# Kernel tuning notes

Measured on AMD Instinct MI355X. Metric: run time of the kernel, lower is better.

## Reference

```python
import jax, jax.numpy as jnp
import numpy as np
import math

D_MODEL = 1024
D_STATE = 16
D_CONV = 4
EXPAND = 2
D_INNER = EXPAND * D_MODEL
DT_RANK = math.ceil(D_MODEL / 16)
EPS = 1e-5


def setup_inputs() -> dict:
    key = jax.random.key(0)
    ks = jax.random.split(key, 8)
    B, L = 2, 1024
    s = 0.02
    return {
        "hidden_states": jax.random.normal(ks[0], (B, L, D_MODEL), jnp.float32),
        "norm_weight": jnp.ones((D_MODEL,), jnp.float32),
        "in_proj_w": (jax.random.normal(ks[1], (2 * D_INNER, D_MODEL), jnp.float32) * s),
        "conv_w": (jax.random.normal(ks[2], (D_INNER, D_CONV), jnp.float32) * s),
        "conv_b": jnp.zeros((D_INNER,), jnp.float32),
        "x_proj_w": (jax.random.normal(ks[3], (DT_RANK + 2 * D_STATE, D_INNER), jnp.float32) * s),
        "dt_proj_w": (jax.random.normal(ks[4], (D_INNER, DT_RANK), jnp.float32) * s),
        "dt_proj_b": jax.random.uniform(ks[5], (D_INNER,), jnp.float32, -4.0, -2.0),
        "A_log": jnp.log(jnp.broadcast_to(jnp.arange(1, D_STATE + 1, dtype=jnp.float32), (D_INNER, D_STATE))),
        "D": jnp.ones((D_INNER,), jnp.float32),
        "out_proj_w": (jax.random.normal(ks[6], (D_MODEL, D_INNER), jnp.float32) * s),
    }


def _rmsnorm(x, w):
    # Faithful to source: rms = ||x||_2 / sqrt(d); x / (rms + eps) * w
    norm = jnp.linalg.norm(x, axis=-1, keepdims=True)
    rms = norm * (1.0 / math.sqrt(x.shape[-1]))
    return w * (x / (rms + EPS))


def _mamba(h, in_proj_w, conv_w, conv_b, x_proj_w, dt_proj_w, dt_proj_b, A_log, D, out_proj_w):
    B, L, _ = h.shape
    xz = h @ in_proj_w.T                      # (B,L,2*D_INNER)
    x, z = jnp.split(xz, 2, axis=-1)          # each (B,L,D_INNER)

    # causal depthwise conv1d along L, kernel D_CONV
    xpad = jnp.pad(x, ((0, 0), (D_CONV - 1, 0), (0, 0)))
    xc = conv_b
    for k in range(D_CONV):                   # tiny fixed loop over kernel taps
        xc = xc + xpad[:, k:k + L, :] * conv_w[:, k]
    xc = jax.nn.silu(xc)                      # (B,L,D_INNER)

    x_dbl = xc @ x_proj_w.T                   # (B,L,DT_RANK+2N)
    dt, Bm, Cm = jnp.split(x_dbl, [DT_RANK, DT_RANK + D_STATE], axis=-1)
    dt = jax.nn.softplus(dt @ dt_proj_w.T + dt_proj_b)   # (B,L,D_INNER)

    A = -jnp.exp(A_log)                       # (D_INNER,N)
    deltaA = jnp.exp(dt[..., None] * A)                      # (B,L,D_INNER,N)
    deltaBu = (dt * xc)[..., None] * Bm[:, :, None, :]        # (B,L,D_INNER,N)

    def step(hst, inp):
        dA, dBu, Ct = inp
        hst = dA * hst + dBu                  # (B,D_INNER,N)
        y = jnp.einsum('bdn,bn->bd', hst, Ct)
        return hst, y

    h0 = jnp.zeros((B, D_INNER, D_STATE), xc.dtype)
    _, ys = jax.lax.scan(step, h0, (deltaA.swapaxes(0, 1), deltaBu.swapaxes(0, 1), Cm.swapaxes(0, 1)))
    y = ys.swapaxes(0, 1)                     # (B,L,D_INNER)
    y = y + D * xc
    y = y * jax.nn.silu(z)
    return y @ out_proj_w.T                   # (B,L,D_MODEL)


def reference(hidden_states, norm_weight, in_proj_w, conv_w, conv_b, x_proj_w,
              dt_proj_w, dt_proj_b, A_log, D, out_proj_w):
    residual = hidden_states
    h = _rmsnorm(residual, norm_weight)
    out = _mamba(h, in_proj_w, conv_w, conv_b, x_proj_w, dt_proj_w, dt_proj_b,
                 A_log, D, out_proj_w)
    return out, residual
```

## Files before the change

### kernel.cpp

```cpp
#include <hip/hip_runtime.h>

typedef __bf16 bf16x8 __attribute__((ext_vector_type(8)));
typedef float f32x4 __attribute__((ext_vector_type(4)));

__device__ __forceinline__ float b2f(ushort u) {
    union { unsigned int i; float f; } v;
    v.i = ((unsigned int)u) << 16;
    return v.f;
}
__device__ __forceinline__ ushort f2b(float f) {
    union { float f; unsigned int i; } v;
    v.f = f;
    unsigned int x = v.i;
    unsigned int r = (x + 0x7fffu + ((x >> 16) & 1u)) >> 16;
    return (ushort)r;
}

#define D_MODEL 1024
#define D_INNER 2048
#define D_STATE 16
#define DT_RANK 64
#define NTOK    2048
#define LSEQ    1024
#define NCH     32
#define LC      32
#define KSL     16

__global__ __launch_bounds__(256) void cvt_bf16_kernel(
    const float* __restrict__ src, ushort* __restrict__ dst, int n4)
{
    int i = blockIdx.x * 256 + threadIdx.x;
    if (i >= n4) return;
    float4 v = *(const float4*)(src + i * 4);
    ushort4 o;
    o.x = f2b(v.x); o.y = f2b(v.y); o.z = f2b(v.z); o.w = f2b(v.w);
    *(ushort4*)(dst + i * 4) = o;
}

__global__ __launch_bounds__(256) void rmsnorm_kernel(
    const float* __restrict__ hs, const float* __restrict__ w,
    ushort* __restrict__ hout, float* __restrict__ resid)
{
    int t = blockIdx.x;
    int tid = threadIdx.x;
    float4 r4 = *(const float4*)(hs + (size_t)t * D_MODEL + tid * 4);
    float s = r4.x * r4.x + r4.y * r4.y + r4.z * r4.z + r4.w * r4.w;
    #pragma unroll
    for (int off = 32; off >= 1; off >>= 1) s += __shfl_xor(s, off);
    __shared__ float red[4];
    int lane = tid & 63, wid = tid >> 6;
    if (lane == 0) red[wid] = s;
    __syncthreads();
    float tot = red[0] + red[1] + red[2] + red[3];
    float inv = 1.0f / (sqrtf(tot) * (1.0f / 32.0f) + 1e-5f);
    float4 w4 = *(const float4*)(w + tid * 4);
    ushort4 o;
    o.x = f2b(w4.x * r4.x * inv);
    o.y = f2b(w4.y * r4.y * inv);
    o.z = f2b(w4.z * r4.z * inv);
    o.w = f2b(w4.w * r4.w * inv);
    *(ushort4*)(hout + (size_t)t * D_MODEL + tid * 4) = o;
    *(float4*)(resid + (size_t)t * D_MODEL + tid * 4) = r4;
}

__global__ __launch_bounds__(256) void gemm_bt_kernel(
    const ushort* __restrict__ Ag, const ushort* __restrict__ Wg,
    float* __restrict__ Cf, int M, int N, int K)
{
    __shared__ __align__(16) ushort sA[128 * 40];
    __shared__ __align__(16) ushort sB[128 * 40];
    int tid = threadIdx.x;
    int bm = blockIdx.x, bn = blockIdx.y;
    int wid = tid >> 6, lane = tid & 63;
    int wm = (wid >> 1) * 64, wn = (wid & 1) * 64;
    int l16 = lane & 15, q = lane >> 4;

    f32x4 acc[4][4];
    #pragma unroll
    for (int i = 0; i < 4; i++)
        #pragma unroll
        for (int j = 0; j < 4; j++)
            acc[i][j] = (f32x4){0.f, 0.f, 0.f, 0.f};

    const ushort* Abase = Ag + (size_t)bm * 128 * K;
    const ushort* Wbase = Wg + (size_t)bn * 128 * K;

    int r0 = tid >> 2, c0 = (tid & 3) << 3;
    const ushort* pA0 = Abase + (size_t)r0 * K + c0;
    const ushort* pA1 = Abase + (size_t)(r0 + 64) * K + c0;
    const ushort* pB0 = Wbase + (size_t)r0 * K + c0;
    const ushort* pB1 = Wbase + (size_t)(r0 + 64) * K + c0;

    uint4 pa0 = *(const uint4*)(pA0), pa1 = *(const uint4*)(pA1);
    uint4 pb0 = *(const uint4*)(pB0), pb1 = *(const uint4*)(pB1);

    for (int k0 = 0; k0 < K; k0 += 32) {
        *(uint4*)(sA + r0 * 40 + c0)        = pa0;
        *(uint4*)(sA + (r0 + 64) * 40 + c0) = pa1;
        *(uint4*)(sB + r0 * 40 + c0)        = pb0;
        *(uint4*)(sB + (r0 + 64) * 40 + c0) = pb1;
        __syncthreads();
        if (k0 + 32 < K) {
            pa0 = *(const uint4*)(pA0 + k0 + 32);
            pa1 = *(const uint4*)(pA1 + k0 + 32);
            pb0 = *(const uint4*)(pB0 + k0 + 32);
            pb1 = *(const uint4*)(pB1 + k0 + 32);
        }
        bf16x8 af[4], bfr[4];
        #pragma unroll
        for (int i = 0; i < 4; i++)
            af[i] = *(const bf16x8*)(sA + (wm + i * 16 + l16) * 40 + q * 8);
        #pragma unroll
        for (int j = 0; j < 4; j++)
            bfr[j] = *(const bf16x8*)(sB + (wn + j * 16 + l16) * 40 + q * 8);
        #pragma unroll
        for (int i = 0; i < 4; i++)
            #pragma unroll
            for (int j = 0; j < 4; j++)
                acc[i][j] = __builtin_amdgcn_mfma_f32_16x16x32_bf16(af[i], bfr[j], acc[i][j], 0, 0, 0);
        __syncthreads();
    }

    int row0 = bm * 128 + wm + q * 4;
    int col0 = bn * 128 + wn + l16;
    #pragma unroll
    for (int i = 0; i < 4; i++)
        #pragma unroll
        for (int j = 0; j < 4; j++)
            #pragma unroll
            for (int r = 0; r < 4; r++)
                Cf[(size_t)(row0 + i * 16 + r) * N + col0 + j * 16] = acc[i][j][r];
}

__global__ __launch_bounds__(256) void gemm64_kernel(
    const ushort* __restrict__ Ag, const ushort* __restrict__ Wg,
    float* __restrict__ Cf, int M, int N, int K)
{
    __shared__ __align__(16) ushort sA[64 * 72];
    __shared__ __align__(16) ushort sB[64 * 72];
    int tid = threadIdx.x;
    int bm = blockIdx.x, bn = blockIdx.y;
    int wid = tid >> 6, lane = tid & 63;
    int wm = wid * 16;
    int l16 = lane & 15, q = lane >> 4;

    f32x4 acc[4];
    #pragma unroll
    for (int j = 0; j < 4; j++) acc[j] = (f32x4){0.f, 0.f, 0.f, 0.f};

    const ushort* Abase = Ag + (size_t)bm * 64 * K;
    const ushort* Wbase = Wg + (size_t)bn * 64 * K;

    int r0 = tid >> 3, c0 = (tid & 7) << 3;
    const ushort* pA0 = Abase + (size_t)r0 * K + c0;
    const ushort* pA1 = Abase + (size_t)(r0 + 32) * K + c0;
    const ushort* pB0 = Wbase + (size_t)r0 * K + c0;
    const ushort* pB1 = Wbase + (size_t)(r0 + 32) * K + c0;

    uint4 pa0 = *(const uint4*)(pA0), pa1 = *(const uint4*)(pA1);
    uint4 pb0 = *(const uint4*)(pB0), pb1 = *(const uint4*)(pB1);

    for (int k0 = 0; k0 < K; k0 += 64) {
        *(uint4*)(sA + r0 * 72 + c0)        = pa0;
        *(uint4*)(sA + (r0 + 32) * 72 + c0) = pa1;
        *(uint4*)(sB + r0 * 72 + c0)        = pb0;
        *(uint4*)(sB + (r0 + 32) * 72 + c0) = pb1;
        __syncthreads();
        if (k0 + 64 < K) {
            pa0 = *(const uint4*)(pA0 + k0 + 64);
            pa1 = *(const uint4*)(pA1 + k0 + 64);
            pb0 = *(const uint4*)(pB0 + k0 + 64);
            pb1 = *(const uint4*)(pB1 + k0 + 64);
        }
        #pragma unroll
        for (int ks = 0; ks < 2; ks++) {
            bf16x8 af = *(const bf16x8*)(sA + (wm + l16) * 72 + ks * 32 + q * 8);
            bf16x8 bfr[4];
            #pragma unroll
            for (int j = 0; j < 4; j++)
                bfr[j] = *(const bf16x8*)(sB + (j * 16 + l16) * 72 + ks * 32 + q * 8);
            #pragma unroll
            for (int j = 0; j < 4; j++)
                acc[j] = __builtin_amdgcn_mfma_f32_16x16x32_bf16(af, bfr[j], acc[j], 0, 0, 0);
        }
        __syncthreads();
    }

    int row0 = bm * 64 + wm + q * 4;
    int col0 = bn * 64 + l16;
    #pragma unroll
    for (int j = 0; j < 4; j++)
        #pragma unroll
        for (int r = 0; r < 4; r++)
            Cf[(size_t)(row0 + r) * N + col0 + j * 16] = acc[j][r];
}

__global__ __launch_bounds__(256) void conv_silu_kernel(
    const float* __restrict__ xz, const float* __restrict__ cw,
    const float* __restrict__ cb, float* __restrict__ xc, ushort* __restrict__ xcb)
{
    int idx = blockIdx.x * 256 + threadIdx.x;
    int d = idx & (D_INNER - 1);
    int t = idx >> 11;
    int l = t & (LSEQ - 1), b = t >> 10;
    float4 w4 = *(const float4*)(cw + d * 4);
    float acc = cb[d];
    float wk[4] = {w4.x, w4.y, w4.z, w4.w};
    #pragma unroll
    for (int k = 0; k < 4; k++) {
        int ll = l - 3 + k;
        float xv = (ll >= 0) ? xz[(((size_t)(b * LSEQ + ll)) << 12) + d] : 0.f;
        acc += xv * wk[k];
    }
    float sg = acc / (1.f + __expf(-acc));
    xc[idx] = sg;
    xcb[idx] = f2b(sg);
}

__global__ __launch_bounds__(256) void xproj_partial_kernel(
    const ushort* __restrict__ xcb, const ushort* __restrict__ wq,
    float* __restrict__ partials)
{
    __shared__ __align__(16) ushort sA[128 * 32];
    __shared__ __align__(16) ushort sB[96 * 32];
    int tid = threadIdx.x;
    int bm = blockIdx.x, sl = blockIdx.y;
    int wid = tid >> 6, lane = tid & 63;
    int wm = wid * 32;
    int l16 = lane & 15, q = lane >> 4;

    f32x4 acc[2][6];
    #pragma unroll
    for (int i = 0; i < 2; i++)
        #pragma unroll
        for (int j = 0; j < 6; j++)
            acc[i][j] = (f32x4){0.f, 0.f, 0.f, 0.f};

    const ushort* Abase = xcb + (size_t)bm * 128 * D_INNER;
    int kbase = sl * (D_INNER / KSL);

    for (int kk = 0; kk < D_INNER / KSL; kk += 32) {
        int k0 = kbase + kk;
        __syncthreads();
        #pragma unroll
        for (int i = tid; i < 512; i += 256) {
            int r = i >> 2, c = (i & 3) << 3;
            *(uint4*)(sA + i * 8) = *(const uint4*)(Abase + (size_t)r * D_INNER + k0 + c);
        }
        for (int i = tid; i < 384; i += 256) {
            int r = i >> 2, c = (i & 3) << 3;
            *(uint4*)(sB + i * 8) = *(const uint4*)(wq + (size_t)r * D_INNER + k0 + c);
        }
        __syncthreads();
        bf16x8 af[2], bfr[6];
        #pragma unroll
        for (int i = 0; i < 2; i++)
            af[i] = *(const bf16x8*)(sA + (wm + i * 16 + l16) * 32 + q * 8);
        #pragma unroll
        for (int j = 0; j < 6; j++)
            bfr[j] = *(const bf16x8*)(sB + (j * 16 + l16) * 32 + q * 8);
        #pragma unroll
        for (int i = 0; i < 2; i++)
            #pragma unroll
            for (int j = 0; j < 6; j++)
                acc[i][j] = __builtin_amdgcn_mfma_f32_16x16x32_bf16(af[i], bfr[j], acc[i][j], 0, 0, 0);
    }

    float* out = partials + (size_t)sl * NTOK * 96;
    int row0 = bm * 128 + wm + q * 4;
    #pragma unroll
    for (int i = 0; i < 2; i++)
        #pragma unroll
        for (int j = 0; j < 6; j++)
            #pragma unroll
            for (int r = 0; r < 4; r++)
                out[(size_t)(row0 + i * 16 + r) * 96 + j * 16 + l16] = acc[i][j][r];
}

__global__ __launch_bounds__(256) void xproj_reduce_kernel(
    const float* __restrict__ partials, float* __restrict__ xdbl,
    ushort* __restrict__ xdbl64)
{
    int idx = blockIdx.x * 256 + threadIdx.x;
    float s = 0.f;
    #pragma unroll
    for (int sl = 0; sl < KSL; sl++)
        s += partials[(size_t)sl * NTOK * 96 + idx];
    xdbl[idx] = s;
    int col = idx % 96;
    if (col < DT_RANK)
        xdbl64[(size_t)(idx / 96) * DT_RANK + col] = f2b(s);
}

__global__ __launch_bounds__(256) void dt_gemm_kernel(
    const ushort* __restrict__ xd64, const ushort* __restrict__ dtwq,
    const float* __restrict__ dtb, ushort* __restrict__ dtout)
{
    __shared__ __align__(16) ushort sA[64 * 72];
    __shared__ __align__(16) ushort sB[64 * 72];
    int tid = threadIdx.x;
    int bm = blockIdx.x, bn = blockIdx.y;
    int wid = tid >> 6, lane = tid & 63;
    int wm = wid * 16;
    int l16 = lane & 15, q = lane >> 4;

    const ushort* Abase = xd64 + (size_t)bm * 64 * DT_RANK;
    const ushort* Bbase = dtwq + (size_t)bn * 64 * DT_RANK;
    #pragma unroll
    for (int i = tid; i < 512; i += 256) {
        int r = i >> 3, c = (i & 7) << 3;
        *(uint4*)(sA + r * 72 + c) = *(const uint4*)(Abase + (size_t)r * DT_RANK + c);
        *(uint4*)(sB + r * 72 + c) = *(const uint4*)(Bbase + (size_t)r * DT_RANK + c);
    }
    __syncthreads();

    f32x4 acc[4];
    #pragma unroll
    for (int j = 0; j < 4; j++) acc[j] = (f32x4){0.f, 0.f, 0.f, 0.f};

    #pragma unroll
    for (int ks = 0; ks < 2; ks++) {
        bf16x8 af = *(const bf16x8*)(sA + (wm + l16) * 72 + ks * 32 + q * 8);
        bf16x8 bfr[4];
        #pragma unroll
        for (int j = 0; j < 4; j++)
            bfr[j] = *(const bf16x8*)(sB + (j * 16 + l16) * 72 + ks * 32 + q * 8);
        #pragma unroll
        for (int j = 0; j < 4; j++)
            acc[j] = __builtin_amdgcn_mfma_f32_16x16x32_bf16(af, bfr[j], acc[j], 0, 0, 0);
    }

    __syncthreads();
    #pragma unroll
    for (int j = 0; j < 4; j++) {
        float bias = dtb[bn * 64 + j * 16 + l16];
        #pragma unroll
        for (int r = 0; r < 4; r++) {
            float s = acc[j][r] + bias;
            float sp = (s > 20.f) ? s : log1pf(__expf(s));
            sA[(wm + q * 4 + r) * 72 + j * 16 + l16] = f2b(sp);
        }
    }
    __syncthreads();
    int row0 = bm * 64, col0 = bn * 64;
    #pragma unroll
    for (int rep = 0; rep < 2; rep++) {
        int off = rep * 2048 + tid * 8;
        int row = off >> 6, col = off & 63;
        *(uint4*)(dtout + (size_t)(row0 + row) * D_INNER + col0 + col) =
            *(const uint4*)(sA + row * 72 + col);
    }
}

__global__ __launch_bounds__(256) void scan_partA_kernel(
    const ushort* __restrict__ dt, const float* __restrict__ xc,
    const float* __restrict__ xdbl, const float* __restrict__ Alog,
    float2* __restrict__ ch1, float2* __restrict__ ch2)
{
    __shared__ float sBC[LC][32];
    int bid = blockIdx.x;
    int g = bid & 7;
    int c = (bid >> 3) & (NCH - 1);
    int b = bid >> 8;
    int tid = threadIdx.x;
    int lane = tid & 63, wid = tid >> 6;
    int d = g * 256 + wid * 64 + lane;
    int l0 = c * LC;

    {
        int r = tid >> 3, c4 = (tid & 7) * 4;
        *(float4*)&sBC[r][c4] =
            *(const float4*)(xdbl + ((size_t)(b * LSEQ + l0 + r)) * 96 + 64 + c4);
    }
    float A[16];
    #pragma unroll
    for (int k = 0; k < 4; k++)
        *(float4*)&A[k * 4] = *(const float4*)(Alog + d * D_STATE + k * 4);
    #pragma unroll
    for (int n = 0; n < 16; n++) A[n] = -__expf(A[n]);
    __syncthreads();

    const ushort* dtp = dt + ((size_t)(b * LSEQ + l0)) * D_INNER + d;
    const float*  xcp = xc + ((size_t)(b * LSEQ + l0)) * D_INNER + d;

    float h[16], ap[16];
    #pragma unroll
    for (int n = 0; n < 16; n++) { h[n] = 0.f; ap[n] = 1.f; }

    for (int l = 0; l < LC; l++) {
        float dtv = b2f(dtp[(size_t)l * D_INNER]);
        float xcv = xcp[(size_t)l * D_INNER];
        float t = dtv * xcv;
        float Bv[16];
        #pragma unroll
        for (int k = 0; k < 4; k++)
            *(float4*)&Bv[k * 4] = *(const float4*)&sBC[l][k * 4];
        #pragma unroll
        for (int n = 0; n < 16; n++) {
            float a = __expf(dtv * A[n]);
            h[n] = h[n] * a + t * Bv[n];
            ap[n] *= a;
        }
    }

    float2* outp = (c < 16 ? ch1 : ch2) +
                   ((size_t)((b * 16 + (c & 15)) * D_INNER + d)) * D_STATE;
    #pragma unroll
    for (int n = 0; n < 16; n += 2) {
        float4 v = {ap[n], h[n], ap[n + 1], h[n + 1]};
        *(float4*)&outp[n] = v;
    }
}

__global__ __launch_bounds__(256) void scan_partB_kernel(
    float2* __restrict__ ch1, float2* __restrict__ ch2)
{
    int kk = blockIdx.x * 256 + threadIdx.x;
    int b = kk >> 15, dn = kk & 32767;
    float run = 0.f;
    #pragma unroll
    for (int c = 0; c < NCH; c++) {
        float2* p = (c < 16 ? ch1 : ch2) +
                    (size_t)(b * 16 + (c & 15)) * 32768 + dn;
        float2 v = *p;
        p->x = run;
        run = v.x * run + v.y;
    }
}

__global__ __launch_bounds__(256) void scan_partC_kernel(
    const ushort* __restrict__ dt, const float* __restrict__ xc,
    const float* __restrict__ xdbl, const float* __restrict__ xz,
    const float* __restrict__ Alog, const float* __restrict__ Dp,
    const float2* __restrict__ ch1, const float2* __restrict__ ch2,
    ushort* __restrict__ yg)
{
    __shared__ float sBC[LC][32];
    int bid = blockIdx.x;
    int g = bid & 7;
    int c = (bid >> 3) & (NCH - 1);
    int b = bid >> 8;
    int tid = threadIdx.x;
    int lane = tid & 63, wid = tid >> 6;
    int d = g * 256 + wid * 64 + lane;
    int l0 = c * LC;

    {
        int r = tid >> 3, c4 = (tid & 7) * 4;
        *(float4*)&sBC[r][c4] =
            *(const float4*)(xdbl + ((size_t)(b * LSEQ + l0 + r)) * 96 + 64 + c4);
    }
    float A[16];
    #pragma unroll
    for (int k = 0; k < 4; k++)
        *(float4*)&A[k * 4] = *(const float4*)(Alog + d * D_STATE + k * 4);
    #pragma unroll
    for (int n = 0; n < 16; n++) A[n] = -__expf(A[n]);
    float Dd = Dp[d];

    const float2* hip_ = (c < 16 ? ch1 : ch2) +
                         ((size_t)((b * 16 + (c & 15)) * D_INNER + d)) * D_STATE;
    float h[16];
    #pragma unroll
    for (int n = 0; n < 16; n += 2) {
        float4 v = *(const float4*)&hip_[n];
        h[n] = v.x; h[n + 1] = v.z;
    }
    __syncthreads();

    const ushort* dtp = dt + ((size_t)(b * LSEQ + l0)) * D_INNER + d;
    const float*  xcp = xc + ((size_t)(b * LSEQ + l0)) * D_INNER + d;
    const float*  zp  = xz + ((size_t)(b * LSEQ + l0)) * (2 * D_INNER) + D_INNER + d;
    ushort* yp = yg + ((size_t)(b * LSEQ + l0)) * D_INNER + d;

    for (int l = 0; l < LC; l++) {
        float dtv = b2f(dtp[(size_t)l * D_INNER]);
        float xcv = xcp[(size_t)l * D_INNER];
        float zv  = zp[(size_t)l * (2 * D_INNER)];
        float t = dtv * xcv;
        float Bv[16], Cv[16];
        #pragma unroll
        for (int k = 0; k < 4; k++) {
            *(float4*)&Bv[k * 4] = *(const float4*)&sBC[l][k * 4];
            *(float4*)&Cv[k * 4] = *(const float4*)&sBC[l][16 + k * 4];
        }
        float p0 = 0.f, p1 = 0.f, p2 = 0.f, p3 = 0.f;
        #pragma unroll
        for (int n = 0; n < 16; n += 4) {
            float a0 = __expf(dtv * A[n]);
            float a1 = __expf(dtv * A[n + 1]);
            float a2 = __expf(dtv * A[n + 2]);
            float a3 = __expf(dtv * A[n + 3]);
            h[n]     = h[n] * a0 + t * Bv[n];
            h[n + 1] = h[n + 1] * a1 + t * Bv[n + 1];
            h[n + 2] = h[n + 2] * a2 + t * Bv[n + 2];
            h[n + 3] = h[n + 3] * a3 + t * Bv[n + 3];
            p0 += h[n] * Cv[n];
            p1 += h[n + 1] * Cv[n + 1];
            p2 += h[n + 2] * Cv[n + 2];
            p3 += h[n + 3] * Cv[n + 3];
        }
        float p = (p0 + p1) + (p2 + p3);
        float y = p + Dd * xcv;
        float sz = zv / (1.f + __expf(-zv));
        yp[(size_t)l * D_INNER] = f2b(y * sz);
    }
}

extern "C" void kernel_launch(void* const* d_in, const int* in_sizes, int n_in,
                              void* d_out, int out_size, void* d_ws, size_t ws_size,
                              hipStream_t stream)
{
    const float* hs      = (const float*)d_in[0];
    const float* norm_w  = (const float*)d_in[1];
    const float* inproj  = (const float*)d_in[2];
    const float* convw   = (const float*)d_in[3];
    const float* convb   = (const float*)d_in[4];
    const float* xprojw  = (const float*)d_in[5];
    const float* dtw     = (const float*)d_in[6];
    const float* dtb     = (const float*)d_in[7];
    const float* alog    = (const float*)d_in[8];
    const float* dvec    = (const float*)d_in[9];
    const float* outproj = (const float*)d_in[10];

    float* out_main  = (float*)d_out;
    float* out_resid = (float*)d_out + (size_t)NTOK * D_MODEL;

    char* ws = (char*)d_ws;
    float*  xz_f32  = (float*)(ws);
    float*  xc_f32  = (float*)(ws + 33554432);
    ushort* dt_bf16 = (ushort*)(ws + 50331648);
    float2* ch1     = (float2*)(ws + 58720256);
    float*  xdbl    = (float*)(ws + 67108864);
    ushort* h_bf16  = (ushort*)(ws + 67895296);
    ushort* yg_bf16 = (ushort*)(ws + 72089600);
    float2* ch2     = (float2*)(ws + 80478208);
    ushort* wIn     = (ushort*)(ws + 80478208);
    ushort* wOut    = (ushort*)(ws + 88866816);
    ushort* xpw_b   = (ushort*)(ws + 67895296);
    ushort* dtw_b   = (ushort*)(ws + 68288512);
    ushort* xd64_b  = (ushort*)(ws + 68550656);
    ushort* xc_bf16 = (ushort*)(ws + 72089600);
    float*  xprojP  = (float*)(ws + 50331648);

    cvt_bf16_kernel<<<(2 * D_INNER * D_MODEL / 4 + 255) / 256, 256, 0, stream>>>(
        inproj, wIn, 2 * D_INNER * D_MODEL / 4);
    cvt_bf16_kernel<<<(D_MODEL * D_INNER / 4 + 255) / 256, 256, 0, stream>>>(
        outproj, wOut, D_MODEL * D_INNER / 4);

    rmsnorm_kernel<<<NTOK, 256, 0, stream>>>(hs, norm_w, h_bf16, out_resid);

    gemm_bt_kernel<<<dim3(NTOK / 128, (2 * D_INNER) / 128), 256, 0, stream>>>(
        h_bf16, wIn, xz_f32, NTOK, 2 * D_INNER, D_MODEL);

    cvt_bf16_kernel<<<(96 * D_INNER / 4 + 255) / 256, 256, 0, stream>>>(
        xprojw, xpw_b, 96 * D_INNER / 4);
    cvt_bf16_kernel<<<(D_INNER * DT_RANK / 4 + 255) / 256, 256, 0, stream>>>(
        dtw, dtw_b, D_INNER * DT_RANK / 4);

    conv_silu_kernel<<<(NTOK * D_INNER) / 256, 256, 0, stream>>>(
        xz_f32, convw, convb, xc_f32, xc_bf16);

    xproj_partial_kernel<<<dim3(NTOK / 128, KSL), 256, 0, stream>>>(
        xc_bf16, xpw_b, xprojP);
    xproj_reduce_kernel<<<NTOK * 96 / 256, 256, 0, stream>>>(xprojP, xdbl, xd64_b);

    dt_gemm_kernel<<<dim3(NTOK / 64, D_INNER / 64), 256, 0, stream>>>(
        xd64_b, dtw_b, dtb, dt_bf16);

    scan_partA_kernel<<<512, 256, 0, stream>>>(dt_bf16, xc_f32, xdbl, alog, ch1, ch2);
    scan_partB_kernel<<<256, 256, 0, stream>>>(ch1, ch2);
    scan_partC_kernel<<<512, 256, 0, stream>>>(dt_bf16, xc_f32, xdbl, xz_f32,
                                               alog, dvec, ch1, ch2, yg_bf16);

    gemm64_kernel<<<dim3(NTOK / 64, D_MODEL / 64), 256, 0, stream>>>(
        yg_bf16, wOut, out_main, NTOK, D_MODEL, D_INNER);
}
```

Baseline: 268.6 us.

## Store xz and conv output in bf16 and merge weight conversion launches

The in-projection GEMM now writes x and z as separate bf16 arrays instead of one fp32 xz buffer. The conv kernel reads bf16 x and emits only the bf16 activation, and both scan kernels read bf16 xc and z. This roughly halves the activation memory traffic between stages and removes the fp32 xc copy. The four weight conversion launches are merged into one kernel. The trade-off is extra rounding error on x, z and xc, and the workspace layout is reorganized.

```diff
diff --git a/kernel.cpp b/kernel.cpp
--- a/kernel.cpp
+++ b/kernel.cpp
@@ -26,15 +26,23 @@
 #define LC      32
 #define KSL     16
 
-__global__ __launch_bounds__(256) void cvt_bf16_kernel(
-    const float* __restrict__ src, ushort* __restrict__ dst, int n4)
+__global__ __launch_bounds__(256) void cvt_all_kernel(
+    const float* __restrict__ inproj, const float* __restrict__ outproj,
+    const float* __restrict__ xprojw, const float* __restrict__ dtw,
+    ushort* __restrict__ wIn, ushort* __restrict__ wOut,
+    ushort* __restrict__ xpw, ushort* __restrict__ dtwb)
 {
     int i = blockIdx.x * 256 + threadIdx.x;
-    if (i >= n4) return;
-    float4 v = *(const float4*)(src + i * 4);
+    const float* src; ushort* dst; int off;
+    if (i < 1048576)      { src = inproj;  dst = wIn;  off = i; }
+    else if (i < 1572864) { src = outproj; dst = wOut; off = i - 1048576; }
+    else if (i < 1622016) { src = xprojw;  dst = xpw;  off = i - 1572864; }
+    else if (i < 1654784) { src = dtw;     dst = dtwb; off = i - 1622016; }
+    else return;
+    float4 v = *(const float4*)(src + (size_t)off * 4);
     ushort4 o;
     o.x = f2b(v.x); o.y = f2b(v.y); o.z = f2b(v.z); o.w = f2b(v.w);
-    *(ushort4*)(dst + i * 4) = o;
+    *(ushort4*)(dst + (size_t)off * 4) = o;
 }
 
 __global__ __launch_bounds__(256) void rmsnorm_kernel(
@@ -63,9 +71,9 @@
     *(float4*)(resid + (size_t)t * D_MODEL + tid * 4) = r4;
 }
 
-__global__ __launch_bounds__(256) void gemm_bt_kernel(
+__global__ __launch_bounds__(256) void gemm_xz_kernel(
     const ushort* __restrict__ Ag, const ushort* __restrict__ Wg,
-    float* __restrict__ Cf, int M, int N, int K)
+    ushort* __restrict__ xq, ushort* __restrict__ zq, int K)
 {
     __shared__ __align__(16) ushort sA[128 * 40];
     __shared__ __align__(16) ushort sB[128 * 40];
@@ -121,15 +129,17 @@
         __syncthreads();
     }
 
+    ushort* dst = (bn < 16) ? xq : zq;
     int row0 = bm * 128 + wm + q * 4;
-    int col0 = bn * 128 + wn + l16;
+    int col0 = (bn & 15) * 128 + wn + l16;
     #pragma unroll
     for (int i = 0; i < 4; i++)
         #pragma unroll
         for (int j = 0; j < 4; j++)
             #pragma unroll
             for (int r = 0; r < 4; r++)
-                Cf[(size_t)(row0 + i * 16 + r) * N + col0 + j * 16] = acc[i][j][r];
+                dst[(size_t)(row0 + i * 16 + r) * D_INNER + col0 + j * 16] =
+                    f2b(acc[i][j][r]);
 }
 
 __global__ __launch_bounds__(256) void gemm64_kernel(
@@ -196,8 +206,8 @@
 }
 
 __global__ __launch_bounds__(256) void conv_silu_kernel(
-    const float* __restrict__ xz, const float* __restrict__ cw,
-    const float* __restrict__ cb, float* __restrict__ xc, ushort* __restrict__ xcb)
+    const ushort* __restrict__ xq, const float* __restrict__ cw,
+    const float* __restrict__ cb, ushort* __restrict__ xcb)
 {
     int idx = blockIdx.x * 256 + threadIdx.x;
     int d = idx & (D_INNER - 1);
@@ -209,11 +219,10 @@
     #pragma unroll
     for (int k = 0; k < 4; k++) {
         int ll = l - 3 + k;
-        float xv = (ll >= 0) ? xz[(((size_t)(b * LSEQ + ll)) << 12) + d] : 0.f;
+        float xv = (ll >= 0) ? b2f(xq[(((size_t)(b * LSEQ + ll)) << 11) + d]) : 0.f;
         acc += xv * wk[k];
     }
     float sg = acc / (1.f + __expf(-acc));
-    xc[idx] = sg;
     xcb[idx] = f2b(sg);
 }
 
@@ -353,7 +362,7 @@
 }
 
 __global__ __launch_bounds__(256) void scan_partA_kernel(
-    const ushort* __restrict__ dt, const float* __restrict__ xc,
+    const ushort* __restrict__ dt, const ushort* __restrict__ xcq,
     const float* __restrict__ xdbl, const float* __restrict__ Alog,
     float2* __restrict__ ch1, float2* __restrict__ ch2)
 {
@@ -380,8 +389,8 @@
     for (int n = 0; n < 16; n++) A[n] = -__expf(A[n]);
     __syncthreads();
 
-    const ushort* dtp = dt + ((size_t)(b * LSEQ + l0)) * D_INNER + d;
-    const float*  xcp = xc + ((size_t)(b * LSEQ + l0)) * D_INNER + d;
+    const ushort* dtp = dt  + ((size_t)(b * LSEQ + l0)) * D_INNER + d;
+    const ushort* xcp = xcq + ((size_t)(b * LSEQ + l0)) * D_INNER + d;
 
     float h[16], ap[16];
     #pragma unroll
@@ -389,7 +398,7 @@
 
     for (int l = 0; l < LC; l++) {
         float dtv = b2f(dtp[(size_t)l * D_INNER]);
-        float xcv = xcp[(size_t)l * D_INNER];
+        float xcv = b2f(xcp[(size_t)l * D_INNER]);
         float t = dtv * xcv;
         float Bv[16];
         #pragma unroll
@@ -429,8 +438,8 @@
 }
 
 __global__ __launch_bounds__(256) void scan_partC_kernel(
-    const ushort* __restrict__ dt, const float* __restrict__ xc,
-    const float* __restrict__ xdbl, const float* __restrict__ xz,
+    const ushort* __restrict__ dt, const ushort* __restrict__ xcq,
+    const float* __restrict__ xdbl, const ushort* __restrict__ zq,
     const float* __restrict__ Alog, const float* __restrict__ Dp,
     const float2* __restrict__ ch1, const float2* __restrict__ ch2,
     ushort* __restrict__ yg)
@@ -468,15 +477,15 @@
     }
     __syncthreads();
 
-    const ushort* dtp = dt + ((size_t)(b * LSEQ + l0)) * D_INNER + d;
-    const float*  xcp = xc + ((size_t)(b * LSEQ + l0)) * D_INNER + d;
-    const float*  zp  = xz + ((size_t)(b * LSEQ + l0)) * (2 * D_INNER) + D_INNER + d;
+    const ushort* dtp = dt  + ((size_t)(b * LSEQ + l0)) * D_INNER + d;
+    const ushort* xcp = xcq + ((size_t)(b * LSEQ + l0)) * D_INNER + d;
+    const ushort* zp  = zq  + ((size_t)(b * LSEQ + l0)) * D_INNER + d;
     ushort* yp = yg + ((size_t)(b * LSEQ + l0)) * D_INNER + d;
 
     for (int l = 0; l < LC; l++) {
         float dtv = b2f(dtp[(size_t)l * D_INNER]);
-        float xcv = xcp[(size_t)l * D_INNER];
-        float zv  = zp[(size_t)l * (2 * D_INNER)];
+        float xcv = b2f(xcp[(size_t)l * D_INNER]);
+        float zv  = b2f(zp[(size_t)l * D_INNER]);
         float t = dtv * xcv;
         float Bv[16], Cv[16];
         #pragma unroll
@@ -527,50 +536,45 @@
     float* out_resid = (float*)d_out + (size_t)NTOK * D_MODEL;
 
     char* ws = (char*)d_ws;
-    float*  xz_f32  = (float*)(ws);
-    float*  xc_f32  = (float*)(ws + 33554432);
-    ushort* dt_bf16 = (ushort*)(ws + 50331648);
-    float2* ch1     = (float2*)(ws + 58720256);
-    float*  xdbl    = (float*)(ws + 67108864);
-    ushort* h_bf16  = (ushort*)(ws + 67895296);
-    ushort* yg_bf16 = (ushort*)(ws + 72089600);
-    float2* ch2     = (float2*)(ws + 80478208);
-    ushort* wIn     = (ushort*)(ws + 80478208);
-    ushort* wOut    = (ushort*)(ws + 88866816);
-    ushort* xpw_b   = (ushort*)(ws + 67895296);
-    ushort* dtw_b   = (ushort*)(ws + 68288512);
-    ushort* xd64_b  = (ushort*)(ws + 68550656);
-    ushort* xc_bf16 = (ushort*)(ws + 72089600);
-    float*  xprojP  = (float*)(ws + 50331648);
-
-    cvt_bf16_kernel<<<(2 * D_INNER * D_MODEL / 4 + 255) / 256, 256, 0, stream>>>(
-        inproj, wIn, 2 * D_INNER * D_MODEL / 4);
-    cvt_bf16_kernel<<<(D_MODEL * D_INNER / 4 + 255) / 256, 256, 0, stream>>>(
-        outproj, wOut, D_MODEL * D_INNER / 4);
+    ushort* xq      = (ushort*)(ws);
+    ushort* zq      = (ushort*)(ws +  9437184);
+    ushort* xcb     = (ushort*)(ws + 18874368);
+    ushort* dtq     = (ushort*)(ws + 28311552);
+    float2* ch1     = (float2*)(ws + 37748736);
+    float2* ch2     = (float2*)(ws + 47185920);
+    float*  xdbl    = (float*) (ws + 56623104);
+    ushort* xd64    = (ushort*)(ws + 57671680);
+    ushort* xpw_b   = (ushort*)(ws + 58195968);
+    ushort* dtw_b   = (ushort*)(ws + 58720256);
+    ushort* wIn     = (ushort*)(ws + 59768832);
+    ushort* wOut    = (ushort*)(ws + 69206016);
+    ushort* h_bf16  = (ushort*)(ws + 74448896);
+    ushort* yg_bf16 = (ushort*)(ws + 18874368);
+    float*  xprojP  = (float*) (ws + 79691776);
+
+    yg_bf16 = (ushort*)(ws + 79691776);
+
+    cvt_all_kernel<<<6464, 256, 0, stream>>>(
+        inproj, outproj, xprojw, dtw, wIn, wOut, xpw_b, dtw_b);
 
     rmsnorm_kernel<<<NTOK, 256, 0, stream>>>(hs, norm_w, h_bf16, out_resid);
 
-    gemm_bt_kernel<<<dim3(NTOK / 128, (2 * D_INNER) / 128), 256, 0, stream>>>(
-        h_bf16, wIn, xz_f32, NTOK, 2 * D_INNER, D_MODEL);
-
-    cvt_bf16_kernel<<<(96 * D_INNER / 4 + 255) / 256, 256, 0, stream>>>(
-        xprojw, xpw_b, 96 * D_INNER / 4);
-    cvt_bf16_kernel<<<(D_INNER * DT_RANK / 4 + 255) / 256, 256, 0, stream>>>(
-        dtw, dtw_b, D_INNER * DT_RANK / 4);
+    gemm_xz_kernel<<<dim3(NTOK / 128, (2 * D_INNER) / 128), 256, 0, stream>>>(
+        h_bf16, wIn, xq, zq, D_MODEL);
 
     conv_silu_kernel<<<(NTOK * D_INNER) / 256, 256, 0, stream>>>(
-        xz_f32, convw, convb, xc_f32, xc_bf16);
+        xq, convw, convb, xcb);
 
     xproj_partial_kernel<<<dim3(NTOK / 128, KSL), 256, 0, stream>>>(
-        xc_bf16, xpw_b, xprojP);
-    xproj_reduce_kernel<<<NTOK * 96 / 256, 256, 0, stream>>>(xprojP, xdbl, xd64_b);
+        xcb, xpw_b, xprojP);
+    xproj_reduce_kernel<<<NTOK * 96 / 256, 256, 0, stream>>>(xprojP, xdbl, xd64);
 
     dt_gemm_kernel<<<dim3(NTOK / 64, D_INNER / 64), 256, 0, stream>>>(
-        xd64_b, dtw_b, dtb, dt_bf16);
-
-    scan_partA_kernel<<<512, 256, 0, stream>>>(dt_bf16, xc_f32, xdbl, alog, ch1, ch2);
+        xd64, dtw_b, dtb, dtq);
+
+    scan_partA_kernel<<<512, 256, 0, stream>>>(dtq, xcb, xdbl, alog, ch1, ch2);
     scan_partB_kernel<<<256, 256, 0, stream>>>(ch1, ch2);
-    scan_partC_kernel<<<512, 256, 0, stream>>>(dt_bf16, xc_f32, xdbl, xz_f32,
+    scan_partC_kernel<<<512, 256, 0, stream>>>(dtq, xcb, xdbl, zq,
                                                alog, dvec, ch1, ch2, yg_bf16);
 
     gemm64_kernel<<<dim3(NTOK / 64, D_MODEL / 64), 256, 0, stream>>>(
```

Result: no change. 265.1 us (-1.3%).
